# Performance work log

Hardware: AMD Instinct MI355X
Metric: run time of the kernel (lower is better)

## Reference

```python
import jax, jax.numpy as jnp
import numpy as np

N_PAIRS = 500000
L = 4          # l_max + 1
S = 4          # number of species
N_MAX = 16     # n_max per l (uniform)
HID = 32       # MLP hidden width


def setup_inputs() -> dict:
    key = jax.random.key(0)
    ks = jax.random.split(key, 6)
    radial_functions = jax.random.normal(ks[0], (N_PAIRS, L * N_MAX), dtype=jnp.float32)
    species = jax.random.randint(ks[1], (N_PAIRS,), 0, S, dtype=jnp.int64)
    # per-(l, species) MLP weights, stored as [L, S, in, out]; 0.3 scale keeps SiLU well-behaved
    W1 = jax.random.normal(ks[2], (L, S, N_MAX, HID), dtype=jnp.float32) * 0.3
    W2 = jax.random.normal(ks[3], (L, S, HID, HID), dtype=jnp.float32) * 0.3
    W3 = jax.random.normal(ks[4], (L, S, HID, HID), dtype=jnp.float32) * 0.3
    W4 = jax.random.normal(ks[5], (L, S, HID, N_MAX), dtype=jnp.float32) * 0.3
    return {"radial_functions": radial_functions, "species": species,
            "W1": W1, "W2": W2, "W3": W3, "W4": W4}


def reference(radial_functions, species, W1, W2, W3, W4):
    # torch.split(radial_functions, n_max_l, dim=1) with uniform n_max_l == reshape
    n = radial_functions.shape[0]
    x = radial_functions.reshape(n, L, N_MAX)              # [N, L, n_max]
    onehot = jax.nn.one_hot(species, S, dtype=x.dtype)      # [N, S]
    out = jnp.zeros_like(x)
    # per-species MLP applied to the rows of that species (gather-MLP-scatter),
    # expressed as dense compute + one-hot masking (S is tiny, MLPs are tiny)
    for s in range(S):
        h = jax.nn.silu(jnp.einsum('nli,lio->nlo', x, W1[:, s]))   # [N, L, 32]
        h = jax.nn.silu(jnp.einsum('nli,lio->nlo', h, W2[:, s]))
        h = jax.nn.silu(jnp.einsum('nli,lio->nlo', h, W3[:, s]))
        y = jnp.einsum('nli,lio->nlo', h, W4[:, s])                # [N, L, n_max]
        out = out + onehot[:, s][:, None, None] * y
    return out  # equivalent to the list of per-l tensors, stacked along axis 1
```

## Files before the change

### kernel.cpp

```cpp
#include <hip/hip_runtime.h>
#include <stdint.h>

typedef unsigned int u32;
typedef unsigned long long u64;

constexpr int L   = 4;
constexpr int S   = 4;
constexpr int NM  = 16;
constexpr int HID = 32;
constexpr int BLK = 256;
constexpr int NFRAG = 7;
constexpr int WF_ENTRIES = L * S * NFRAG * 64;
constexpr int WS_PERM_INT = (256 + WF_ENTRIES * 16) / 4;

typedef short  s16x8  __attribute__((ext_vector_type(8)));
typedef float  f32x16 __attribute__((ext_vector_type(16)));
typedef float  f32x4  __attribute__((ext_vector_type(4)));
typedef unsigned int u32x2 __attribute__((ext_vector_type(2)));


__device__ __forceinline__ int load_species(const int* sp, int i64, int n) {
    return i64 ? sp[2 * n] : sp[n];
}

__global__ void k_wprep(const void* __restrict__ W1, const void* __restrict__ W2,
                        const void* __restrict__ W3, const void* __restrict__ W4,
                        const u32* __restrict__ rfw, int* __restrict__ hdr,
                        uint4* __restrict__ wf) {
    __shared__ int sf32;
    int tid = threadIdx.x;
    if (tid < 64) {
        u32 w  = rfw[tid];
        u32 lo = w & 0xffffu;
        u32 ex = (lo >> 7) & 0xffu;
        int plausible = (lo == 0u || (ex >= 90u && ex <= 141u)) ? 1 : 0;
        u64 pm = __ballot(plausible);
        if (tid == 0) sf32 = (__popcll(pm) < 48) ? 1 : 0;
    }
    if (blockIdx.x == 0 && tid < 9) hdr[tid] = 0;
    __syncthreads();
    int isf32 = sf32;

    int e = blockIdx.x * BLK + tid;
    if (e >= WF_ENTRIES) return;
    int lam = e & 63;
    int f   = (e >> 6) % NFRAG;
    int ls  = e / (64 * NFRAG);
    int m = lam & 31, h = lam >> 5;
    unsigned short vals[8];
#pragma unroll
    for (int j = 0; j < 8; j++) {
        int k = 8 * h + j;
        const void* base; size_t off; bool zero = false;
        if (f == 0)      { base = W1; off = (size_t)ls * 512  + (size_t)k * 32 + m; }
        else if (f <= 2) { base = W2; off = (size_t)ls * 1024 + (size_t)(k + 16 * (f - 1)) * 32 + m; }
        else if (f <= 4) { base = W3; off = (size_t)ls * 1024 + (size_t)(k + 16 * (f - 3)) * 32 + m; }
        else             { zero = (m >= NM); base = W4;
                           off = (size_t)ls * 512 + (size_t)(k + 16 * (f - 5)) * NM + (m & 15); }
        unsigned short v;
        if (zero) v = 0;
        else if (isf32) {
            u32 u = __float_as_uint(((const float*)base)[off]);
            u32 r = ((u >> 16) & 1u) + 0x7fffu;
            v = (unsigned short)((u + r) >> 16);
        } else v = ((const unsigned short*)base)[off];
        vals[j] = v;
    }
    uint4 q;
    q.x = vals[0] | ((u32)vals[1] << 16);
    q.y = vals[2] | ((u32)vals[3] << 16);
    q.z = vals[4] | ((u32)vals[5] << 16);
    q.w = vals[6] | ((u32)vals[7] << 16);
    wf[e] = q;
}

__global__ void k1_hist(const int* __restrict__ sp, int* __restrict__ hdr, int N) {
    __shared__ int cnt[S];
    __shared__ int si64;
    int t = threadIdx.x;
    if (t < 64) {
        u64 om = __ballot(((const u32*)sp)[2 * t + 1] != 0u);
        if (t == 0) si64 = (om == 0ull) ? 1 : 0;
    }
    if (t < S) cnt[t] = 0;
    __syncthreads();
    int n = blockIdx.x * BLK + t;
    if (n < N) atomicAdd(&cnt[load_species(sp, si64, n)], 1);
    __syncthreads();
    if (t < S) atomicAdd(&hdr[t], cnt[t]);
}

__global__ void k3_scatter(const int* __restrict__ sp, int* __restrict__ hdr,
                           int* __restrict__ perm, int N) {
    __shared__ int cnt[S];
    __shared__ int base[S];
    __shared__ int bp[S + 1];
    __shared__ int cs[S];
    __shared__ int si64;
    int t = threadIdx.x;
    if (t < 64) {
        u64 om = __ballot(((const u32*)sp)[2 * t + 1] != 0u);
        if (t == 0) si64 = (om == 0ull) ? 1 : 0;
    }
    if (t == 0) {
        int acc = 0;
        for (int q = 0; q < S; q++) {
            cs[q] = hdr[q];
            bp[q] = acc;
            acc += (cs[q] + BLK - 1) & ~(BLK - 1);
        }
        bp[S] = acc;
    }
    if (t < S) cnt[t] = 0;
    __syncthreads();
    int i64 = si64;
    int n = blockIdx.x * BLK + t;
    int s = 0, r = 0;
    bool valid = (n < N);
    if (valid) {
        s = load_species(sp, i64, n);
        r = atomicAdd(&cnt[s], 1);
    }
    __syncthreads();
    if (t < S) base[t] = bp[t] + atomicAdd(&hdr[4 + t], cnt[t]);
    __syncthreads();
    if (valid) perm[base[s] + r] = n;
    if (blockIdx.x == 0) {
        for (int q = 0; q < S; q++)
            for (int i = bp[q] + cs[q] + t; i < bp[q + 1]; i += BLK) perm[i] = -1;
    }
}

__device__ __forceinline__ u32 pack_bf16_hu(float a, float b) {
    u32 ua = __float_as_uint(a) + 0x8000u;
    u32 ub = __float_as_uint(b) + 0x8000u;
    return (ua >> 16) | (ub & 0xffff0000u);
}

__device__ __forceinline__ float silu(float v) {
    float e = __expf(-v);
    return v * __builtin_amdgcn_rcpf(1.0f + e);
}

__device__ __forceinline__ void d_to_b(const f32x16& d, s16x8& Ba, s16x8& Bb) {
    u32 P[8];
#pragma unroll
    for (int i = 0; i < 8; i++)
        P[i] = pack_bf16_hu(silu(d[2 * i]), silu(d[2 * i + 1]));
    u32x2 r02 = __builtin_amdgcn_permlane32_swap(P[0], P[2], false, false);
    u32x2 r13 = __builtin_amdgcn_permlane32_swap(P[1], P[3], false, false);
    u32x2 r46 = __builtin_amdgcn_permlane32_swap(P[4], P[6], false, false);
    u32x2 r57 = __builtin_amdgcn_permlane32_swap(P[5], P[7], false, false);
    Ba = __builtin_bit_cast(s16x8, make_uint4(r02[0], r13[0], r02[1], r13[1]));
    Bb = __builtin_bit_cast(s16x8, make_uint4(r46[0], r57[0], r46[1], r57[1]));
}

__device__ __forceinline__ s16x8 bf16pack4(uint4 q0, uint4 q1) {
    u32 w0 = pack_bf16_hu(__uint_as_float(q0.x), __uint_as_float(q0.y));
    u32 w1 = pack_bf16_hu(__uint_as_float(q0.z), __uint_as_float(q0.w));
    u32 w2 = pack_bf16_hu(__uint_as_float(q1.x), __uint_as_float(q1.y));
    u32 w3 = pack_bf16_hu(__uint_as_float(q1.z), __uint_as_float(q1.w));
    return __builtin_bit_cast(s16x8, make_uint4(w0, w1, w2, w3));
}

constexpr int SCW = 36;

__global__ __launch_bounds__(BLK, 3) void k4_mlp(
    const void* __restrict__ rf, const int* __restrict__ hdr,
    const int* __restrict__ perm, const uint4* __restrict__ wf,
    void* __restrict__ outp)
{
    __shared__ uint4 lw[L * NFRAG * 64];
    __shared__ float sc[4][32 * SCW];
    __shared__ int   sn[4][2][32];
    __shared__ int   sf32;

    int tid = threadIdx.x;

    int c0 = hdr[0], c1 = hdr[1], c2 = hdr[2], c3 = hdr[3];
    int b1 = (c0 + BLK - 1) & ~(BLK - 1);
    int b2 = b1 + ((c1 + BLK - 1) & ~(BLK - 1));
    int b3 = b2 + ((c2 + BLK - 1) & ~(BLK - 1));
    int b4 = b3 + ((c3 + BLK - 1) & ~(BLK - 1));
    int p0 = blockIdx.x * BLK;
    if (p0 >= b4) return;
    int s = (p0 >= b3) ? 3 : ((p0 >= b2) ? 2 : ((p0 >= b1) ? 1 : 0));
    s = __builtin_amdgcn_readfirstlane(s);

    if (tid < 64) {
        u32 w  = ((const u32*)rf)[tid];
        u32 lo = w & 0xffffu;
        u32 ex = (lo >> 7) & 0xffu;
        int plausible = (lo == 0u || (ex >= 90u && ex <= 141u)) ? 1 : 0;
        u64 pm = __ballot(plausible);
        if (tid == 0) sf32 = (__popcll(pm) < 48) ? 1 : 0;
    }

#pragma unroll
    for (int c = 0; c < 7; c++) {
        int idx = tid + c * BLK;
        int l = idx / (NFRAG * 64);
        int r = idx - l * (NFRAG * 64);
        lw[idx] = wf[(size_t)((l * S + s) * NFRAG) * 64 + r];
    }

    int wv   = tid >> 6;
    int lane = tid & 63;
    int col  = lane & 31;
    int h    = lane >> 5;

    int n_t[2];
#pragma unroll
    for (int t = 0; t < 2; t++) {
        n_t[t] = perm[p0 + wv * 64 + t * 32 + col];
        sn[wv][t][col] = n_t[t];
    }
    __syncthreads();
    int isf32 = sf32;

    if (isf32) {
        const char* xb = (const char*)rf;
        int nn0 = n_t[0] < 0 ? 0 : n_t[0];
        int nn1 = n_t[1] < 0 ? 0 : n_t[1];
        const uint4* rp0 = (const uint4*)(xb + (size_t)nn0 * 256 + h * 32);
        const uint4* rp1 = (const uint4*)(xb + (size_t)nn1 * 256 + h * 32);

        int rg = lane >> 3;
        int cc = lane & 7;
        float* scb = &sc[wv][0];

        uint4 rawb[2][4];
        rawb[0][0] = rp0[0]; rawb[0][1] = rp0[1];
        rawb[0][2] = rp0[4]; rawb[0][3] = rp0[5];

#pragma unroll
        for (int j = 0; j < 4; j++) {
            int lp = j >> 1, t = j & 1;
            if (j < 3) {
                int jn = j + 1;
                int lpn = jn >> 1, tn = jn & 1;
                const uint4* pl = tn ? rp1 : rp0;
                rawb[jn & 1][0] = pl[lpn * 8 + 0];
                rawb[jn & 1][1] = pl[lpn * 8 + 1];
                rawb[jn & 1][2] = pl[lpn * 8 + 4];
                rawb[jn & 1][3] = pl[lpn * 8 + 5];
            }
            int lA = 2 * lp, lB = 2 * lp + 1;
            s16x8 frA[NFRAG], frB[NFRAG];
#pragma unroll
            for (int f = 0; f < NFRAG; f++) {
                frA[f] = __builtin_bit_cast(s16x8, lw[(lA * NFRAG + f) * 64 + lane]);
                frB[f] = __builtin_bit_cast(s16x8, lw[(lB * NFRAG + f) * 64 + lane]);
            }

            s16x8 B1A = bf16pack4(rawb[j & 1][0], rawb[j & 1][1]);
            s16x8 B1B = bf16pack4(rawb[j & 1][2], rawb[j & 1][3]);

            f32x16 z = {0.0f};
            f32x16 dA = __builtin_amdgcn_mfma_f32_32x32x16_bf16(frA[0], B1A, z, 0, 0, 0);
            f32x16 dB = __builtin_amdgcn_mfma_f32_32x32x16_bf16(frB[0], B1B, z, 0, 0, 0);

            s16x8 BaA, BbA, BaB, BbB;
            d_to_b(dA, BaA, BbA);
            d_to_b(dB, BaB, BbB);
            dA = __builtin_amdgcn_mfma_f32_32x32x16_bf16(frA[1], BaA, z, 0, 0, 0);
            dB = __builtin_amdgcn_mfma_f32_32x32x16_bf16(frB[1], BaB, z, 0, 0, 0);
            dA = __builtin_amdgcn_mfma_f32_32x32x16_bf16(frA[2], BbA, dA, 0, 0, 0);
            dB = __builtin_amdgcn_mfma_f32_32x32x16_bf16(frB[2], BbB, dB, 0, 0, 0);

            d_to_b(dA, BaA, BbA);
            d_to_b(dB, BaB, BbB);
            dA = __builtin_amdgcn_mfma_f32_32x32x16_bf16(frA[3], BaA, z, 0, 0, 0);
            dB = __builtin_amdgcn_mfma_f32_32x32x16_bf16(frB[3], BaB, z, 0, 0, 0);
            dA = __builtin_amdgcn_mfma_f32_32x32x16_bf16(frA[4], BbA, dA, 0, 0, 0);
            dB = __builtin_amdgcn_mfma_f32_32x32x16_bf16(frB[4], BbB, dB, 0, 0, 0);

            d_to_b(dA, BaA, BbA);
            d_to_b(dB, BaB, BbB);
            dA = __builtin_amdgcn_mfma_f32_32x32x16_bf16(frA[5], BaA, z, 0, 0, 0);
            dB = __builtin_amdgcn_mfma_f32_32x32x16_bf16(frB[5], BaB, z, 0, 0, 0);
            dA = __builtin_amdgcn_mfma_f32_32x32x16_bf16(frA[6], BbA, dA, 0, 0, 0);
            dB = __builtin_amdgcn_mfma_f32_32x32x16_bf16(frB[6], BbB, dB, 0, 0, 0);

            float* swA = scb + col * SCW + 4 * h;
            *(f32x4*)swA        = (f32x4){dA[0], dA[1], dA[2], dA[3]};
            *(f32x4*)(swA + 8)  = (f32x4){dA[4], dA[5], dA[6], dA[7]};
            float* swB = swA + 16;
            *(f32x4*)swB        = (f32x4){dB[0], dB[1], dB[2], dB[3]};
            *(f32x4*)(swB + 8)  = (f32x4){dB[4], dB[5], dB[6], dB[7]};

            asm volatile("s_waitcnt lgkmcnt(0)" ::: "memory");
            __builtin_amdgcn_sched_barrier(0);

#pragma unroll
            for (int i = 0; i < 4; i++) {
                int r = 8 * i + rg;
                int n = sn[wv][t][r];
                const float* srd = scb + r * SCW + 4 * cc;
                f32x4 v = *(const f32x4*)srd;
                if (n >= 0)
                    *(f32x4*)((char*)outp + (size_t)n * 256 + (size_t)lp * 128 + cc * 16) = v;
            }
            asm volatile("s_waitcnt lgkmcnt(0)" ::: "memory");
            __builtin_amdgcn_sched_barrier(0);
        }
    } else {
#pragma unroll
        for (int l = 0; l < L; l++) {
            s16x8 fr[NFRAG];
#pragma unroll
            for (int f = 0; f < NFRAG; f++)
                fr[f] = __builtin_bit_cast(s16x8, lw[(l * NFRAG + f) * 64 + lane]);

#pragma unroll
            for (int t = 0; t < 2; t++) {
                int n = n_t[t];
                int nn = n < 0 ? 0 : n;

                const char* xb = (const char*)rf;
                s16x8 B1 = __builtin_bit_cast(s16x8,
                     *(const uint4*)(xb + (size_t)nn * 128 + l * 32 + h * 16));

                f32x16 z = {0.0f};
                f32x16 d1 = __builtin_amdgcn_mfma_f32_32x32x16_bf16(fr[0], B1, z, 0, 0, 0);

                s16x8 Ba, Bb;
                d_to_b(d1, Ba, Bb);
                f32x16 d2 = __builtin_amdgcn_mfma_f32_32x32x16_bf16(fr[1], Ba, z, 0, 0, 0);
                d2 = __builtin_amdgcn_mfma_f32_32x32x16_bf16(fr[2], Bb, d2, 0, 0, 0);

                d_to_b(d2, Ba, Bb);
                f32x16 d3 = __builtin_amdgcn_mfma_f32_32x32x16_bf16(fr[3], Ba, z, 0, 0, 0);
                d3 = __builtin_amdgcn_mfma_f32_32x32x16_bf16(fr[4], Bb, d3, 0, 0, 0);

                d_to_b(d3, Ba, Bb);
                f32x16 d4 = __builtin_amdgcn_mfma_f32_32x32x16_bf16(fr[5], Ba, z, 0, 0, 0);
                d4 = __builtin_amdgcn_mfma_f32_32x32x16_bf16(fr[6], Bb, d4, 0, 0, 0);

                u32 P[4];
#pragma unroll
                for (int i = 0; i < 4; i++) P[i] = pack_bf16_hu(d4[2 * i], d4[2 * i + 1]);
                u32x2 r02 = __builtin_amdgcn_permlane32_swap(P[0], P[2], false, false);
                u32x2 r13 = __builtin_amdgcn_permlane32_swap(P[1], P[3], false, false);
                if (n >= 0) {
                    uint4 v = make_uint4(r02[0], r13[0], r02[1], r13[1]);
                    char* ob = (char*)outp;
                    *(uint4*)(ob + (size_t)n * 128 + l * 32 + h * 16) = v;
                }
            }
        }
    }
}

extern "C" void kernel_launch(void* const* d_in, const int* in_sizes, int n_in,
                              void* d_out, int out_size, void* d_ws, size_t ws_size,
                              hipStream_t stream) {
    const void* rf     = d_in[0];
    const int* species = (const int*)d_in[1];
    const void* W1     = d_in[2];
    const void* W2     = d_in[3];
    const void* W3     = d_in[4];
    const void* W4     = d_in[5];

    int N = in_sizes[1];
    int* hdr   = (int*)d_ws;
    uint4* wf  = (uint4*)((char*)d_ws + 256);
    int* perm  = (int*)d_ws + WS_PERM_INT;

    int nb    = (N + BLK - 1) / BLK;
    int nwp   = (WF_ENTRIES + BLK - 1) / BLK;
    int grid4 = (N + S * (BLK - 1) + BLK - 1) / BLK;

    k_wprep   <<<dim3(nwp),  dim3(BLK), 0, stream>>>(W1, W2, W3, W4,
                                                     (const u32*)rf, hdr, wf);
    k1_hist   <<<dim3(nb),   dim3(BLK), 0, stream>>>(species, hdr, N);
    k3_scatter<<<dim3(nb),   dim3(BLK), 0, stream>>>(species, hdr, perm, N);
    k4_mlp    <<<dim3(grid4),dim3(BLK), 0, stream>>>(rf, hdr, perm, wf, d_out);
}
```

Baseline: 304.9 us.

## Vectorize species loads, use hardware bf16 convert, raise MLP occupancy

The histogram and scatter kernels now have each thread handle four pairs through vector int4 loads, which cuts block count and per-element load overhead. Manual round-half-up bf16 packing is replaced with the v_cvt_pk_bf16_f32 instruction, which rounds to nearest-even. The MLP kernel halves its LDS output staging buffer by writing results out in two 16-row passes. It also raises launch bounds from 3 to 4 blocks per SIMD so more blocks can be resident. The trade-offs are extra waitcnt/barrier rounds in the store path and tighter register limits.

```diff
diff --git a/kernel.cpp b/kernel.cpp
--- a/kernel.cpp
+++ b/kernel.cpp
@@ -84,8 +84,26 @@
     }
     if (t < S) cnt[t] = 0;
     __syncthreads();
-    int n = blockIdx.x * BLK + t;
-    if (n < N) atomicAdd(&cnt[load_species(sp, si64, n)], 1);
+    int i64 = si64;
+    int base = blockIdx.x * (BLK * 4) + t * 4;
+    if (base + 3 < N) {
+        int s0, s1, s2, s3;
+        if (i64) {
+            int4 a = ((const int4*)sp)[base / 2];
+            int4 b = ((const int4*)sp)[base / 2 + 1];
+            s0 = a.x; s1 = a.z; s2 = b.x; s3 = b.z;
+        } else {
+            int4 a = ((const int4*)sp)[base / 4];
+            s0 = a.x; s1 = a.y; s2 = a.z; s3 = a.w;
+        }
+        atomicAdd(&cnt[s0], 1); atomicAdd(&cnt[s1], 1);
+        atomicAdd(&cnt[s2], 1); atomicAdd(&cnt[s3], 1);
+    } else {
+        for (int k = 0; k < 4; k++) {
+            int n = base + k;
+            if (n < N) atomicAdd(&cnt[load_species(sp, i64, n)], 1);
+        }
+    }
     __syncthreads();
     if (t < S) atomicAdd(&hdr[t], cnt[t]);
 }
@@ -114,27 +132,45 @@
     if (t < S) cnt[t] = 0;
     __syncthreads();
     int i64 = si64;
-    int n = blockIdx.x * BLK + t;
-    int s = 0, r = 0;
-    bool valid = (n < N);
-    if (valid) {
-        s = load_species(sp, i64, n);
-        r = atomicAdd(&cnt[s], 1);
-    }
+    int nb0 = blockIdx.x * (BLK * 4) + t * 4;
+    int s_[4], r_[4];
+    bool v_[4];
+    if (nb0 + 3 < N) {
+        if (i64) {
+            int4 a = ((const int4*)sp)[nb0 / 2];
+            int4 b = ((const int4*)sp)[nb0 / 2 + 1];
+            s_[0] = a.x; s_[1] = a.z; s_[2] = b.x; s_[3] = b.z;
+        } else {
+            int4 a = ((const int4*)sp)[nb0 / 4];
+            s_[0] = a.x; s_[1] = a.y; s_[2] = a.z; s_[3] = a.w;
+        }
+        v_[0] = v_[1] = v_[2] = v_[3] = true;
+    } else {
+        for (int k = 0; k < 4; k++) {
+            int n = nb0 + k;
+            v_[k] = (n < N);
+            s_[k] = v_[k] ? load_species(sp, i64, n) : 0;
+        }
+    }
+#pragma unroll
+    for (int k = 0; k < 4; k++)
+        if (v_[k]) r_[k] = atomicAdd(&cnt[s_[k]], 1);
     __syncthreads();
     if (t < S) base[t] = bp[t] + atomicAdd(&hdr[4 + t], cnt[t]);
     __syncthreads();
-    if (valid) perm[base[s] + r] = n;
+#pragma unroll
+    for (int k = 0; k < 4; k++)
+        if (v_[k]) perm[base[s_[k]] + r_[k]] = nb0 + k;
     if (blockIdx.x == 0) {
         for (int q = 0; q < S; q++)
             for (int i = bp[q] + cs[q] + t; i < bp[q + 1]; i += BLK) perm[i] = -1;
     }
 }
 
-__device__ __forceinline__ u32 pack_bf16_hu(float a, float b) {
-    u32 ua = __float_as_uint(a) + 0x8000u;
-    u32 ub = __float_as_uint(b) + 0x8000u;
-    return (ua >> 16) | (ub & 0xffff0000u);
+__device__ __forceinline__ u32 cvt_pk_bf16(float a, float b) {
+    u32 r;
+    asm("v_cvt_pk_bf16_f32 %0, %1, %2" : "=v"(r) : "v"(a), "v"(b));
+    return r;
 }
 
 __device__ __forceinline__ float silu(float v) {
@@ -146,7 +182,7 @@
     u32 P[8];
 #pragma unroll
     for (int i = 0; i < 8; i++)
-        P[i] = pack_bf16_hu(silu(d[2 * i]), silu(d[2 * i + 1]));
+        P[i] = cvt_pk_bf16(silu(d[2 * i]), silu(d[2 * i + 1]));
     u32x2 r02 = __builtin_amdgcn_permlane32_swap(P[0], P[2], false, false);
     u32x2 r13 = __builtin_amdgcn_permlane32_swap(P[1], P[3], false, false);
     u32x2 r46 = __builtin_amdgcn_permlane32_swap(P[4], P[6], false, false);
@@ -156,22 +192,22 @@
 }
 
 __device__ __forceinline__ s16x8 bf16pack4(uint4 q0, uint4 q1) {
-    u32 w0 = pack_bf16_hu(__uint_as_float(q0.x), __uint_as_float(q0.y));
-    u32 w1 = pack_bf16_hu(__uint_as_float(q0.z), __uint_as_float(q0.w));
-    u32 w2 = pack_bf16_hu(__uint_as_float(q1.x), __uint_as_float(q1.y));
-    u32 w3 = pack_bf16_hu(__uint_as_float(q1.z), __uint_as_float(q1.w));
+    u32 w0 = cvt_pk_bf16(__uint_as_float(q0.x), __uint_as_float(q0.y));
+    u32 w1 = cvt_pk_bf16(__uint_as_float(q0.z), __uint_as_float(q0.w));
+    u32 w2 = cvt_pk_bf16(__uint_as_float(q1.x), __uint_as_float(q1.y));
+    u32 w3 = cvt_pk_bf16(__uint_as_float(q1.z), __uint_as_float(q1.w));
     return __builtin_bit_cast(s16x8, make_uint4(w0, w1, w2, w3));
 }
 
 constexpr int SCW = 36;
 
-__global__ __launch_bounds__(BLK, 3) void k4_mlp(
+__global__ __launch_bounds__(BLK, 4) void k4_mlp(
     const void* __restrict__ rf, const int* __restrict__ hdr,
     const int* __restrict__ perm, const uint4* __restrict__ wf,
     void* __restrict__ outp)
 {
     __shared__ uint4 lw[L * NFRAG * 64];
-    __shared__ float sc[4][32 * SCW];
+    __shared__ float sc[4][16 * SCW];
     __shared__ int   sn[4][2][32];
     __shared__ int   sf32;
 
@@ -227,6 +263,8 @@
 
         int rg = lane >> 3;
         int cc = lane & 7;
+        int bh = col >> 4;
+        int pr = col & 15;
         float* scb = &sc[wv][0];
 
         uint4 rawb[2][4];
@@ -282,27 +320,32 @@
             dA = __builtin_amdgcn_mfma_f32_32x32x16_bf16(frA[6], BbA, dA, 0, 0, 0);
             dB = __builtin_amdgcn_mfma_f32_32x32x16_bf16(frB[6], BbB, dB, 0, 0, 0);
 
-            float* swA = scb + col * SCW + 4 * h;
-            *(f32x4*)swA        = (f32x4){dA[0], dA[1], dA[2], dA[3]};
-            *(f32x4*)(swA + 8)  = (f32x4){dA[4], dA[5], dA[6], dA[7]};
-            float* swB = swA + 16;
-            *(f32x4*)swB        = (f32x4){dB[0], dB[1], dB[2], dB[3]};
-            *(f32x4*)(swB + 8)  = (f32x4){dB[4], dB[5], dB[6], dB[7]};
-
-            asm volatile("s_waitcnt lgkmcnt(0)" ::: "memory");
-            __builtin_amdgcn_sched_barrier(0);
-
-#pragma unroll
-            for (int i = 0; i < 4; i++) {
-                int r = 8 * i + rg;
-                int n = sn[wv][t][r];
-                const float* srd = scb + r * SCW + 4 * cc;
-                f32x4 v = *(const f32x4*)srd;
-                if (n >= 0)
-                    *(f32x4*)((char*)outp + (size_t)n * 256 + (size_t)lp * 128 + cc * 16) = v;
+#pragma unroll
+            for (int b = 0; b < 2; b++) {
+                if (bh == b) {
+                    float* swA = scb + pr * SCW + 4 * h;
+                    *(f32x4*)swA        = (f32x4){dA[0], dA[1], dA[2], dA[3]};
+                    *(f32x4*)(swA + 8)  = (f32x4){dA[4], dA[5], dA[6], dA[7]};
+                    float* swB = swA + 16;
+                    *(f32x4*)swB        = (f32x4){dB[0], dB[1], dB[2], dB[3]};
+                    *(f32x4*)(swB + 8)  = (f32x4){dB[4], dB[5], dB[6], dB[7]};
+                }
+                asm volatile("s_waitcnt lgkmcnt(0)" ::: "memory");
+                __builtin_amdgcn_sched_barrier(0);
+
+#pragma unroll
+                for (int i = 0; i < 2; i++) {
+                    int lr = 8 * i + rg;
+                    int r  = 16 * b + lr;
+                    int n  = sn[wv][t][r];
+                    const float* srd = scb + lr * SCW + 4 * cc;
+                    f32x4 v = *(const f32x4*)srd;
+                    if (n >= 0)
+                        *(f32x4*)((char*)outp + (size_t)n * 256 + (size_t)lp * 128 + cc * 16) = v;
+                }
+                asm volatile("s_waitcnt lgkmcnt(0)" ::: "memory");
+                __builtin_amdgcn_sched_barrier(0);
             }
-            asm volatile("s_waitcnt lgkmcnt(0)" ::: "memory");
-            __builtin_amdgcn_sched_barrier(0);
         }
     } else {
 #pragma unroll
@@ -339,7 +382,7 @@
 
                 u32 P[4];
 #pragma unroll
-                for (int i = 0; i < 4; i++) P[i] = pack_bf16_hu(d4[2 * i], d4[2 * i + 1]);
+                for (int i = 0; i < 4; i++) P[i] = cvt_pk_bf16(d4[2 * i], d4[2 * i + 1]);
                 u32x2 r02 = __builtin_amdgcn_permlane32_swap(P[0], P[2], false, false);
                 u32x2 r13 = __builtin_amdgcn_permlane32_swap(P[1], P[3], false, false);
                 if (n >= 0) {
@@ -367,13 +410,13 @@
     uint4* wf  = (uint4*)((char*)d_ws + 256);
     int* perm  = (int*)d_ws + WS_PERM_INT;
 
-    int nb    = (N + BLK - 1) / BLK;
+    int nb4   = (N + BLK * 4 - 1) / (BLK * 4);
     int nwp   = (WF_ENTRIES + BLK - 1) / BLK;
     int grid4 = (N + S * (BLK - 1) + BLK - 1) / BLK;
 
     k_wprep   <<<dim3(nwp),  dim3(BLK), 0, stream>>>(W1, W2, W3, W4,
                                                      (const u32*)rf, hdr, wf);
-    k1_hist   <<<dim3(nb),   dim3(BLK), 0, stream>>>(species, hdr, N);
-    k3_scatter<<<dim3(nb),   dim3(BLK), 0, stream>>>(species, hdr, perm, N);
+    k1_hist   <<<dim3(nb4),  dim3(BLK), 0, stream>>>(species, hdr, N);
+    k3_scatter<<<dim3(nb4),  dim3(BLK), 0, stream>>>(species, hdr, perm, N);
     k4_mlp    <<<dim3(grid4),dim3(BLK), 0, stream>>>(rf, hdr, perm, wf, d_out);
 }
```

Measured after the change: 273.0 us. -10.5%, faster.
